# Kernel tuning notes

Hardware: AMD Instinct MI355X
Metric: run time of the kernel (lower is better)

Reference implementation:

```python
import jax, jax.numpy as jnp
import numpy as np

N_NODES = 50000


def gcn_conv(x, src, dst, W, b, n_nodes):
    # PyG GCNConv: add self-loops, symmetric normalization D^-1/2 (A+I) D^-1/2 (x W) + b
    E = src.shape[0]
    deg = jax.ops.segment_sum(jnp.ones((E,), x.dtype), dst, num_segments=n_nodes) + 1.0
    dinv = jax.lax.rsqrt(deg)
    h = x @ W  # [N, H]
    norm = dinv[src] * dinv[dst]  # [E]
    agg = jax.ops.segment_sum(h[src] * norm[:, None], dst, num_segments=n_nodes)
    agg = agg + h * (dinv * dinv)[:, None]  # self-loop contribution
    return agg + b


def setup_inputs() -> dict:
    key = jax.random.key(0)
    ks = jax.random.split(key, 16)
    N, E, D, H, T, O = N_NODES, 800000, 128, 128, 2, 1
    x = jax.random.normal(ks[0], (N, D), jnp.float32)
    edge_index = jax.random.randint(ks[1], (2, E), 0, N, jnp.int32)
    edge_attrs = jax.random.uniform(ks[2], (T, E, 7), jnp.float32)
    s = lambda k, sh: jax.random.normal(k, sh, jnp.float32) * (1.0 / np.sqrt(sh[0]))
    return {
        "x": x, "edge_index": edge_index, "edge_attrs": edge_attrs,
        "W1": s(ks[3], (D, H)), "b1": jnp.zeros((H,), jnp.float32),
        "W2": s(ks[4], (H, H)), "b2": jnp.zeros((H,), jnp.float32),
        "W3": s(ks[5], (H, H)), "b3": jnp.zeros((H,), jnp.float32),
        "We": s(ks[6], (2 * H + 7, H)), "be": jnp.zeros((H,), jnp.float32),
        "Wg": s(ks[7], (H, O)), "bg": jnp.zeros((O,), jnp.float32),
    }


def reference(x, edge_index, edge_attrs, W1, b1, W2, b2, W3, b3, We, be, Wg, bg):
    src, dst = edge_index[0], edge_index[1]
    n = x.shape[0]
    outputs = []
    for t in range(edge_attrs.shape[0]):  # small fixed T, x evolves across iterations
        edge_attr = edge_attrs[t]
        x = jax.nn.relu(gcn_conv(x, src, dst, W1, b1, n))
        x = jax.nn.relu(gcn_conv(x, src, dst, W2, b2, n))
        x = jax.nn.relu(gcn_conv(x, src, dst, W3, b3, n))
        # gather-concat-MLP-mean per edge
        edge_features = jnp.concatenate([x[src], x[dst], edge_attr], axis=1)
        edge_output = jax.nn.relu(edge_features @ We + be)
        graph_features = jnp.mean(edge_output, axis=0, keepdims=True)  # [1, H]
        outputs.append(graph_features @ Wg + bg)
        W1 = W2  # no-op placeholder removed below
        W1 = W1  # keep W1 unchanged
    return jnp.concatenate(outputs, axis=0)  # [T, output_dim]
```

## Files before the change

kernel.cpp:

```cpp
#include <hip/hip_runtime.h>
#include <hip/hip_bf16.h>


typedef __attribute__((ext_vector_type(8))) short bf16x8;
typedef __attribute__((ext_vector_type(4))) float f32x4;
typedef __attribute__((ext_vector_type(2))) float f32x2;

__device__ __forceinline__ unsigned short f2bf(float f) {
    union { float f; unsigned int u; } v; v.f = f;
    unsigned int r = v.u + 0x7fffu + ((v.u >> 16) & 1u);
    return (unsigned short)(r >> 16);
}
__device__ __forceinline__ float bf2f(unsigned short h) {
    union { unsigned int u; float f; } v; v.u = ((unsigned int)h) << 16;
    return v.f;
}
__device__ __forceinline__ unsigned int pk2bf(float lo, float hi) {
    return (unsigned int)f2bf(lo) | ((unsigned int)f2bf(hi) << 16);
}
__device__ __forceinline__ unsigned char f2fp8(float f) {
    return (unsigned char)(__builtin_amdgcn_cvt_pk_fp8_f32(f, f, 0, false) & 0xff);
}
__device__ __forceinline__ void fp8x4(unsigned int u, float* o) {
    f32x2 lo = __builtin_amdgcn_cvt_pk_f32_fp8(u, false);
    f32x2 hi = __builtin_amdgcn_cvt_pk_f32_fp8(u, true);
    o[0] = lo[0]; o[1] = lo[1]; o[2] = hi[0]; o[3] = hi[1];
}
__device__ __forceinline__ void de16add(uint4 v, float* a) {
    float t[4];
    fp8x4(v.x, t); a[0]+=t[0]; a[1]+=t[1]; a[2]+=t[2]; a[3]+=t[3];
    fp8x4(v.y, t); a[4]+=t[0]; a[5]+=t[1]; a[6]+=t[2]; a[7]+=t[3];
    fp8x4(v.z, t); a[8]+=t[0]; a[9]+=t[1]; a[10]+=t[2]; a[11]+=t[3];
    fp8x4(v.w, t); a[12]+=t[0]; a[13]+=t[1]; a[14]+=t[2]; a[15]+=t[3];
}

__global__ void to_bf16(const float* __restrict__ in, unsigned short* __restrict__ out, int n4)
{
    int i = blockIdx.x * 256 + threadIdx.x;
    if (i < n4) {
        float4 v = ((const float4*)in)[i];
        ushort4 o;
        o.x = f2bf(v.x); o.y = f2bf(v.y); o.z = f2bf(v.z); o.w = f2bf(v.w);
        ((ushort4*)out)[i] = o;
    }
}

__global__ void transpose_w(
    const float* __restrict__ W1, const float* __restrict__ W2,
    const float* __restrict__ W3, const float* __restrict__ We,
    unsigned short* __restrict__ T1, unsigned short* __restrict__ T2,
    unsigned short* __restrict__ T3, unsigned short* __restrict__ Tuv)
{
    const float* src; unsigned short* dst;
    switch (blockIdx.y) {
        case 0:  src = W1;             dst = T1;              break;
        case 1:  src = W2;             dst = T2;              break;
        case 2:  src = W3;             dst = T3;              break;
        case 3:  src = We;             dst = Tuv;             break;
        default: src = We + 128 * 128; dst = Tuv + 128 * 128; break;
    }
    for (int i = blockIdx.x * 256 + threadIdx.x; i < 128 * 128; i += 256 * gridDim.x) {
        int k = i >> 7, c = i & 127;
        dst[c * 128 + k] = f2bf(src[i]);
    }
}

__global__ __launch_bounds__(256) void mfma_matmul(
    const unsigned short* __restrict__ X, const unsigned short* __restrict__ Wt,
    unsigned char* __restrict__ out, const float* __restrict__ scale,
    int n_rows, int out_stride, int out_off)
{
    if (blockIdx.y) { Wt += 128 * 128; out_off += 128; }

    const int wave = threadIdx.x >> 6;
    const int lane = threadIdx.x & 63;
    const int m = lane & 15;
    const int q = lane >> 4;
    const int r = blockIdx.x * 64 + wave * 16 + m;
    const bool rv = r < n_rows;

    f32x4 acc[8];
    #pragma unroll
    for (int i = 0; i < 8; ++i) acc[i] = (f32x4){0.f, 0.f, 0.f, 0.f};

    #pragma unroll
    for (int k0 = 0; k0 < 128; k0 += 32) {
        bf16x8 a = {};
        if (rv) a = *(const bf16x8*)(X + (size_t)r * 128 + k0 + q * 8);
        #pragma unroll
        for (int ct = 0; ct < 8; ++ct) {
            bf16x8 b = *(const bf16x8*)(Wt + (ct * 16 + m) * 128 + k0 + q * 8);
            acc[ct] = __builtin_amdgcn_mfma_f32_16x16x32_bf16(a, b, acc[ct], 0, 0, 0);
        }
    }

    #pragma unroll
    for (int reg = 0; reg < 4; ++reg) {
        int gr = blockIdx.x * 64 + wave * 16 + q * 4 + reg;
        if (gr >= n_rows) continue;
        float s = scale ? scale[gr] : 1.0f;
        #pragma unroll
        for (int ct = 0; ct < 8; ++ct) {
            out[(size_t)gr * out_stride + out_off + ct * 16 + m] =
                f2fp8(acc[ct][reg] * s);
        }
    }
}

__global__ __launch_bounds__(256) void gcn_gather(
    const unsigned char* __restrict__ hs, const int* __restrict__ csr_src,
    const int* __restrict__ offs, const int* __restrict__ counts,
    const float* __restrict__ dinv, const float* __restrict__ bias,
    unsigned short* __restrict__ xout, int n)
{
    int node = blockIdx.x * 32 + (threadIdx.x >> 3);
    if (node >= n) return;
    int lane = threadIdx.x & 7;
    int c16 = lane * 16;
    int off = offs[node];
    int cnt = counts[node];

    float a[16] = {};
    de16add(*(const uint4*)(hs + (size_t)node * 128 + c16), a);

    int j = 0;
    for (; j + 8 <= cnt; j += 8) {
        int s0 = csr_src[off + j + 0];
        int s1 = csr_src[off + j + 1];
        int s2 = csr_src[off + j + 2];
        int s3 = csr_src[off + j + 3];
        int s4 = csr_src[off + j + 4];
        int s5 = csr_src[off + j + 5];
        int s6 = csr_src[off + j + 6];
        int s7 = csr_src[off + j + 7];
        uint4 h0 = *(const uint4*)(hs + (size_t)s0 * 128 + c16);
        uint4 h1 = *(const uint4*)(hs + (size_t)s1 * 128 + c16);
        uint4 h2 = *(const uint4*)(hs + (size_t)s2 * 128 + c16);
        uint4 h3 = *(const uint4*)(hs + (size_t)s3 * 128 + c16);
        uint4 h4 = *(const uint4*)(hs + (size_t)s4 * 128 + c16);
        uint4 h5 = *(const uint4*)(hs + (size_t)s5 * 128 + c16);
        uint4 h6 = *(const uint4*)(hs + (size_t)s6 * 128 + c16);
        uint4 h7 = *(const uint4*)(hs + (size_t)s7 * 128 + c16);
        de16add(h0, a); de16add(h1, a); de16add(h2, a); de16add(h3, a);
        de16add(h4, a); de16add(h5, a); de16add(h6, a); de16add(h7, a);
    }
    for (; j + 4 <= cnt; j += 4) {
        int s0 = csr_src[off + j + 0];
        int s1 = csr_src[off + j + 1];
        int s2 = csr_src[off + j + 2];
        int s3 = csr_src[off + j + 3];
        uint4 h0 = *(const uint4*)(hs + (size_t)s0 * 128 + c16);
        uint4 h1 = *(const uint4*)(hs + (size_t)s1 * 128 + c16);
        uint4 h2 = *(const uint4*)(hs + (size_t)s2 * 128 + c16);
        uint4 h3 = *(const uint4*)(hs + (size_t)s3 * 128 + c16);
        de16add(h0, a); de16add(h1, a); de16add(h2, a); de16add(h3, a);
    }
    for (; j < cnt; ++j) {
        int s = csr_src[off + j];
        de16add(*(const uint4*)(hs + (size_t)s * 128 + c16), a);
    }

    float dn = dinv[node];
    float r[16];
    #pragma unroll
    for (int i = 0; i < 4; ++i) {
        float4 bb = *(const float4*)(bias + c16 + i * 4);
        r[i*4+0] = fmaxf(fmaf(a[i*4+0], dn, bb.x), 0.f);
        r[i*4+1] = fmaxf(fmaf(a[i*4+1], dn, bb.y), 0.f);
        r[i*4+2] = fmaxf(fmaf(a[i*4+2], dn, bb.z), 0.f);
        r[i*4+3] = fmaxf(fmaf(a[i*4+3], dn, bb.w), 0.f);
    }
    uint4 o0, o1;
    o0.x = pk2bf(r[0], r[1]);  o0.y = pk2bf(r[2], r[3]);
    o0.z = pk2bf(r[4], r[5]);  o0.w = pk2bf(r[6], r[7]);
    o1.x = pk2bf(r[8], r[9]);  o1.y = pk2bf(r[10], r[11]);
    o1.z = pk2bf(r[12], r[13]); o1.w = pk2bf(r[14], r[15]);
    *(uint4*)(xout + (size_t)node * 128 + c16) = o0;
    *(uint4*)(xout + (size_t)node * 128 + c16 + 8) = o1;
}

#define EM_CHUNK 256
__global__ __launch_bounds__(256) void edge_mlp(
    const unsigned char* __restrict__ uv, const int* __restrict__ src,
    const int* __restrict__ dst, const float* __restrict__ ea,
    const float* __restrict__ We_e, const float* __restrict__ be,
    const float* __restrict__ Wg, float* __restrict__ acc, int E)
{
    const int tid  = threadIdx.x;
    const int lane = tid & 31;
    const int g    = tid >> 5;
    const int c4   = lane * 4;

    __shared__ float eas[EM_CHUNK * 7];
    __shared__ int   ss[EM_CHUNK];
    __shared__ int   ds[EM_CHUNK];
    __shared__ float red[256];

    float4 w[7];
    #pragma unroll
    for (int i = 0; i < 7; ++i)
        w[i] = *(const float4*)(We_e + i * 128 + c4);
    const float4 be4 = *(const float4*)(be + c4);
    const float4 wg4 = *(const float4*)(Wg + c4);

    float4 part = make_float4(0.f, 0.f, 0.f, 0.f);

    for (int base = blockIdx.x * EM_CHUNK; base < E; base += gridDim.x * EM_CHUNK) {
        const int nch = min(EM_CHUNK, E - base);
        for (int i = tid; i < nch * 7; i += 256)
            eas[i] = ea[(size_t)base * 7 + i];
        for (int i = tid; i < nch; i += 256) {
            ss[i] = src[base + i];
            ds[i] = dst[base + i];
        }
        __syncthreads();

        auto ev = [&](int j) {
            unsigned int us = *(const unsigned int*)(uv + (size_t)ss[j] * 256 + c4);
            unsigned int vs = *(const unsigned int*)(uv + (size_t)ds[j] * 256 + 128 + c4);
            float uf[4], vf[4];
            fp8x4(us, uf); fp8x4(vs, vf);
            const float* eav = &eas[j * 7];
            float4 val;
            val.x = uf[0] + vf[0] + be4.x;
            val.y = uf[1] + vf[1] + be4.y;
            val.z = uf[2] + vf[2] + be4.z;
            val.w = uf[3] + vf[3] + be4.w;
            #pragma unroll
            for (int i = 0; i < 7; ++i) {
                float e = eav[i];
                val.x = fmaf(e, w[i].x, val.x);
                val.y = fmaf(e, w[i].y, val.y);
                val.z = fmaf(e, w[i].z, val.z);
                val.w = fmaf(e, w[i].w, val.w);
            }
            part.x += fmaxf(val.x, 0.f);
            part.y += fmaxf(val.y, 0.f);
            part.z += fmaxf(val.z, 0.f);
            part.w += fmaxf(val.w, 0.f);
        };

        int j = g;
        for (; j + 32 <= nch; j += 32) {
            ev(j); ev(j + 8); ev(j + 16); ev(j + 24);
        }
        for (; j < nch; j += 8)
            ev(j);
        __syncthreads();
    }

    float p = part.x * wg4.x + part.y * wg4.y + part.z * wg4.z + part.w * wg4.w;
    red[tid] = p;
    __syncthreads();
    for (int s = 128; s > 0; s >>= 1) {
        if (tid < s) red[tid] += red[tid + s];
        __syncthreads();
    }
    if (tid == 0) atomicAdd(acc, red[0]);
}

__global__ void count_edges(const int* __restrict__ dst, int* __restrict__ counts, int E)
{
    int e = blockIdx.x * 256 + threadIdx.x;
    if (e < E) atomicAdd(&counts[dst[e]], 1);
}

__global__ void compute_dinv(const int* __restrict__ counts, float* __restrict__ dinv, int n)
{
    int i = blockIdx.x * 256 + threadIdx.x;
    if (i < n) dinv[i] = rsqrtf((float)counts[i] + 1.0f);
}

__global__ void scan1(const int* __restrict__ counts, int* __restrict__ scanned,
                      int* __restrict__ btot, int n)
{
    __shared__ int sh[256];
    int i = blockIdx.x * 256 + threadIdx.x;
    int v = (i < n) ? counts[i] : 0;
    sh[threadIdx.x] = v;
    __syncthreads();
    for (int off = 1; off < 256; off <<= 1) {
        int t = (threadIdx.x >= off) ? sh[threadIdx.x - off] : 0;
        __syncthreads();
        sh[threadIdx.x] += t;
        __syncthreads();
    }
    if (i < n) scanned[i] = sh[threadIdx.x] - v;
    if (threadIdx.x == 255) btot[blockIdx.x] = sh[255];
}

__global__ void scan2(int* __restrict__ btot, int nb)
{
    __shared__ int sh[256];
    int v = (threadIdx.x < nb) ? btot[threadIdx.x] : 0;
    sh[threadIdx.x] = v;
    __syncthreads();
    for (int off = 1; off < 256; off <<= 1) {
        int t = (threadIdx.x >= off) ? sh[threadIdx.x - off] : 0;
        __syncthreads();
        sh[threadIdx.x] += t;
        __syncthreads();
    }
    if (threadIdx.x < nb) btot[threadIdx.x] = sh[threadIdx.x] - v;
}

__global__ void scan3(const int* __restrict__ scanned, const int* __restrict__ btot,
                      int* __restrict__ offs, int* __restrict__ cursor, int n)
{
    int i = blockIdx.x * 256 + threadIdx.x;
    if (i < n) {
        int o = scanned[i] + btot[blockIdx.x];
        offs[i] = o;
        cursor[i] = o;
    }
}

__global__ void fill_csr(const int* __restrict__ src, const int* __restrict__ dst,
                         int* __restrict__ cursor, int* __restrict__ csr_src, int E)
{
    int e = blockIdx.x * 256 + threadIdx.x;
    if (e < E) {
        int slot = atomicAdd(&cursor[dst[e]], 1);
        csr_src[slot] = src[e];
    }
}

__global__ void write_out(const float* __restrict__ acc, const float* __restrict__ bg,
                          float* __restrict__ out, float invE, int T)
{
    int t = threadIdx.x;
    if (t < T) out[t] = acc[t] * invE + bg[0];
}


extern "C" void kernel_launch(void* const* d_in, const int* in_sizes, int n_in,
                              void* d_out, int out_size, void* d_ws, size_t ws_size,
                              hipStream_t stream)
{
    const float* x   = (const float*)d_in[0];
    const int*  eidx = (const int*)d_in[1];
    const float* ea  = (const float*)d_in[2];
    const float* W1  = (const float*)d_in[3];
    const float* b1  = (const float*)d_in[4];
    const float* W2  = (const float*)d_in[5];
    const float* b2  = (const float*)d_in[6];
    const float* W3  = (const float*)d_in[7];
    const float* b3  = (const float*)d_in[8];
    const float* We  = (const float*)d_in[9];
    const float* be  = (const float*)d_in[10];
    const float* Wg  = (const float*)d_in[11];
    const float* bg  = (const float*)d_in[12];

    const int N = in_sizes[0] / 128;
    const int E = in_sizes[1] / 2;
    const int T = in_sizes[2] / (E * 7);
    const int* src = eidx;
    const int* dst = eidx + E;

    char* wsp = (char*)d_ws;
    auto alloc = [&](size_t bytes) -> char* {
        char* p = wsp;
        wsp += (bytes + 255) / 256 * 256;
        return p;
    };
    int*   counts  = (int*)alloc((size_t)N * 4);
    int*   offs    = (int*)alloc((size_t)N * 4);
    int*   cursor  = (int*)alloc((size_t)N * 4);
    int*   scanned = (int*)alloc((size_t)N * 4);
    int*   btot    = (int*)alloc(1024);
    int*   csr_src = (int*)alloc((size_t)E * 4);
    float* dinv    = (float*)alloc((size_t)N * 4);
    float* acc     = (float*)alloc(256);
    unsigned short* X0 = (unsigned short*)alloc((size_t)N * 128 * 2);
    unsigned short* A  = (unsigned short*)alloc((size_t)N * 128 * 2);
    unsigned char*  B  = (unsigned char*)alloc((size_t)N * 256);
    unsigned short* T1 = (unsigned short*)alloc(128 * 128 * 2);
    unsigned short* T2 = (unsigned short*)alloc(128 * 128 * 2);
    unsigned short* T3 = (unsigned short*)alloc(128 * 128 * 2);
    unsigned short* Tuv = (unsigned short*)alloc(256 * 128 * 2);

    hipMemsetAsync(counts, 0, (size_t)N * 4, stream);
    hipMemsetAsync(acc, 0, (size_t)T * 4, stream);

    to_bf16<<<(N * 128 / 4 + 255) / 256, 256, 0, stream>>>(x, X0, N * 128 / 4);
    transpose_w<<<dim3(4, 5), 256, 0, stream>>>(W1, W2, W3, We, T1, T2, T3, Tuv);

    count_edges<<<(E + 255) / 256, 256, 0, stream>>>(dst, counts, E);
    compute_dinv<<<(N + 255) / 256, 256, 0, stream>>>(counts, dinv, N);
    const int nb = (N + 255) / 256;
    scan1<<<nb, 256, 0, stream>>>(counts, scanned, btot, N);
    scan2<<<1, 256, 0, stream>>>(btot, nb);
    scan3<<<nb, 256, 0, stream>>>(scanned, btot, offs, cursor, N);
    fill_csr<<<(E + 255) / 256, 256, 0, stream>>>(src, dst, cursor, csr_src, E);

    const int mmb = (N + 63) / 64;
    const int ngb = (N + 31) / 32;
    const int emb = (E + EM_CHUNK - 1) / EM_CHUNK;

    for (int t = 0; t < T; ++t) {
        const unsigned short* xin = (t == 0) ? X0 : A;
        const unsigned short* Tc1 = (t == 0) ? T1 : T2;
        mfma_matmul<<<dim3(mmb, 1), 256, 0, stream>>>(xin, Tc1, B, dinv, N, 128, 0);
        gcn_gather<<<ngb, 256, 0, stream>>>(B, csr_src, offs, counts, dinv, b1, A, N);
        mfma_matmul<<<dim3(mmb, 1), 256, 0, stream>>>(A, T2, B, dinv, N, 128, 0);
        gcn_gather<<<ngb, 256, 0, stream>>>(B, csr_src, offs, counts, dinv, b2, A, N);
        mfma_matmul<<<dim3(mmb, 1), 256, 0, stream>>>(A, T3, B, dinv, N, 128, 0);
        gcn_gather<<<ngb, 256, 0, stream>>>(B, csr_src, offs, counts, dinv, b3, A, N);
        mfma_matmul<<<dim3(mmb, 2), 256, 0, stream>>>(A, Tuv, B, nullptr, N, 256, 0);
        edge_mlp<<<emb, 256, 0, stream>>>(B, src, dst, ea + (size_t)t * E * 7,
                                          We + 256 * 128, be, Wg, acc + t, E);
    }
    write_out<<<1, 64, 0, stream>>>(acc, bg, (float*)d_out, 1.0f / (float)E, T);
}
```

Before: 671.6 us.

## Fuse GCN gather with the next layer's matmul via shared-memory tile

Each GCN aggregation kernel now writes its bf16 activations for a 64-node tile into LDS and immediately multiplies by the next layer's weights with MFMA. This removes the bf16 activation round trip through global memory and cuts the separate matmul launches. The third layer also computes the next timestep's first-layer projection alongside the edge projections, using an extended weight buffer that holds a W2 copy. The trade-offs are lower gather parallelism per block (64 nodes per block, each thread handling two nodes), an MFMA loop that reloads weights for each column tile, and fewer independent waves hiding gather latency.

```diff
diff --git a/kernel.cpp b/kernel.cpp
--- a/kernel.cpp
+++ b/kernel.cpp
@@ -10,10 +10,6 @@
     union { float f; unsigned int u; } v; v.f = f;
     unsigned int r = v.u + 0x7fffu + ((v.u >> 16) & 1u);
     return (unsigned short)(r >> 16);
-}
-__device__ __forceinline__ float bf2f(unsigned short h) {
-    union { unsigned int u; float f; } v; v.u = ((unsigned int)h) << 16;
-    return v.f;
 }
 __device__ __forceinline__ unsigned int pk2bf(float lo, float hi) {
     return (unsigned int)f2bf(lo) | ((unsigned int)f2bf(hi) << 16);
@@ -53,11 +49,12 @@
 {
     const float* src; unsigned short* dst;
     switch (blockIdx.y) {
-        case 0:  src = W1;             dst = T1;              break;
-        case 1:  src = W2;             dst = T2;              break;
-        case 2:  src = W3;             dst = T3;              break;
-        case 3:  src = We;             dst = Tuv;             break;
-        default: src = We + 128 * 128; dst = Tuv + 128 * 128; break;
+        case 0:  src = W1;             dst = T1;               break;
+        case 1:  src = W2;             dst = T2;               break;
+        case 2:  src = W3;             dst = T3;               break;
+        case 3:  src = We;             dst = Tuv;              break;
+        case 4:  src = We + 128 * 128; dst = Tuv + 128 * 128;  break;
+        default: src = W2;             dst = Tuv + 256 * 128;  break;
     }
     for (int i = blockIdx.x * 256 + threadIdx.x; i < 128 * 128; i += 256 * gridDim.x) {
         int k = i >> 7, c = i & 127;
@@ -67,11 +64,8 @@
 
 __global__ __launch_bounds__(256) void mfma_matmul(
     const unsigned short* __restrict__ X, const unsigned short* __restrict__ Wt,
-    unsigned char* __restrict__ out, const float* __restrict__ scale,
-    int n_rows, int out_stride, int out_off)
-{
-    if (blockIdx.y) { Wt += 128 * 128; out_off += 128; }
-
+    unsigned char* __restrict__ out, const float* __restrict__ scale, int n_rows)
+{
     const int wave = threadIdx.x >> 6;
     const int lane = threadIdx.x & 63;
     const int m = lane & 15;
@@ -98,85 +92,92 @@
     for (int reg = 0; reg < 4; ++reg) {
         int gr = blockIdx.x * 64 + wave * 16 + q * 4 + reg;
         if (gr >= n_rows) continue;
-        float s = scale ? scale[gr] : 1.0f;
+        float s = scale[gr];
         #pragma unroll
-        for (int ct = 0; ct < 8; ++ct) {
-            out[(size_t)gr * out_stride + out_off + ct * 16 + m] =
-                f2fp8(acc[ct][reg] * s);
-        }
-    }
-}
-
-__global__ __launch_bounds__(256) void gcn_gather(
-    const unsigned char* __restrict__ hs, const int* __restrict__ csr_src,
+        for (int ct = 0; ct < 8; ++ct)
+            out[(size_t)gr * 128 + ct * 16 + m] = f2fp8(acc[ct][reg] * s);
+    }
+}
+
+#define FPAD 136
+__global__ __launch_bounds__(256) void fused_gm(
+    const unsigned char* __restrict__ hs_in, const int* __restrict__ csr_src,
     const int* __restrict__ offs, const int* __restrict__ counts,
     const float* __restrict__ dinv, const float* __restrict__ bias,
-    unsigned short* __restrict__ xout, int n)
-{
-    int node = blockIdx.x * 32 + (threadIdx.x >> 3);
-    if (node >= n) return;
-    int lane = threadIdx.x & 7;
-    int c16 = lane * 16;
-    int off = offs[node];
-    int cnt = counts[node];
-
-    float a[16] = {};
-    de16add(*(const uint4*)(hs + (size_t)node * 128 + c16), a);
-
-    int j = 0;
-    for (; j + 8 <= cnt; j += 8) {
-        int s0 = csr_src[off + j + 0];
-        int s1 = csr_src[off + j + 1];
-        int s2 = csr_src[off + j + 2];
-        int s3 = csr_src[off + j + 3];
-        int s4 = csr_src[off + j + 4];
-        int s5 = csr_src[off + j + 5];
-        int s6 = csr_src[off + j + 6];
-        int s7 = csr_src[off + j + 7];
-        uint4 h0 = *(const uint4*)(hs + (size_t)s0 * 128 + c16);
-        uint4 h1 = *(const uint4*)(hs + (size_t)s1 * 128 + c16);
-        uint4 h2 = *(const uint4*)(hs + (size_t)s2 * 128 + c16);
-        uint4 h3 = *(const uint4*)(hs + (size_t)s3 * 128 + c16);
-        uint4 h4 = *(const uint4*)(hs + (size_t)s4 * 128 + c16);
-        uint4 h5 = *(const uint4*)(hs + (size_t)s5 * 128 + c16);
-        uint4 h6 = *(const uint4*)(hs + (size_t)s6 * 128 + c16);
-        uint4 h7 = *(const uint4*)(hs + (size_t)s7 * 128 + c16);
-        de16add(h0, a); de16add(h1, a); de16add(h2, a); de16add(h3, a);
-        de16add(h4, a); de16add(h5, a); de16add(h6, a); de16add(h7, a);
-    }
-    for (; j + 4 <= cnt; j += 4) {
-        int s0 = csr_src[off + j + 0];
-        int s1 = csr_src[off + j + 1];
-        int s2 = csr_src[off + j + 2];
-        int s3 = csr_src[off + j + 3];
-        uint4 h0 = *(const uint4*)(hs + (size_t)s0 * 128 + c16);
-        uint4 h1 = *(const uint4*)(hs + (size_t)s1 * 128 + c16);
-        uint4 h2 = *(const uint4*)(hs + (size_t)s2 * 128 + c16);
-        uint4 h3 = *(const uint4*)(hs + (size_t)s3 * 128 + c16);
-        de16add(h0, a); de16add(h1, a); de16add(h2, a); de16add(h3, a);
-    }
-    for (; j < cnt; ++j) {
-        int s = csr_src[off + j];
-        de16add(*(const uint4*)(hs + (size_t)s * 128 + c16), a);
-    }
-
-    float dn = dinv[node];
-    float r[16];
+    const unsigned short* __restrict__ Wt, int ncols, int uvcols,
+    unsigned char* __restrict__ buv, unsigned char* __restrict__ bh, int n)
+{
+    __shared__ unsigned short xs[64 * FPAD];
+    const int tid = threadIdx.x;
+
     #pragma unroll
-    for (int i = 0; i < 4; ++i) {
-        float4 bb = *(const float4*)(bias + c16 + i * 4);
-        r[i*4+0] = fmaxf(fmaf(a[i*4+0], dn, bb.x), 0.f);
-        r[i*4+1] = fmaxf(fmaf(a[i*4+1], dn, bb.y), 0.f);
-        r[i*4+2] = fmaxf(fmaf(a[i*4+2], dn, bb.z), 0.f);
-        r[i*4+3] = fmaxf(fmaf(a[i*4+3], dn, bb.w), 0.f);
-    }
-    uint4 o0, o1;
-    o0.x = pk2bf(r[0], r[1]);  o0.y = pk2bf(r[2], r[3]);
-    o0.z = pk2bf(r[4], r[5]);  o0.w = pk2bf(r[6], r[7]);
-    o1.x = pk2bf(r[8], r[9]);  o1.y = pk2bf(r[10], r[11]);
-    o1.z = pk2bf(r[12], r[13]); o1.w = pk2bf(r[14], r[15]);
-    *(uint4*)(xout + (size_t)node * 128 + c16) = o0;
-    *(uint4*)(xout + (size_t)node * 128 + c16 + 8) = o1;
+    for (int half = 0; half < 2; ++half) {
+        int row  = half * 32 + (tid >> 3);
+        int node = blockIdx.x * 64 + row;
+        if (node < n) {
+            int c16 = (tid & 7) * 16;
+            int off = offs[node];
+            int cnt = counts[node];
+
+            float a[16] = {};
+            de16add(*(const uint4*)(hs_in + (size_t)node * 128 + c16), a);
+            int j = 0;
+            for (; j + 4 <= cnt; j += 4) {
+                int s0 = csr_src[off + j + 0];
+                int s1 = csr_src[off + j + 1];
+                int s2 = csr_src[off + j + 2];
+                int s3 = csr_src[off + j + 3];
+                uint4 h0 = *(const uint4*)(hs_in + (size_t)s0 * 128 + c16);
+                uint4 h1 = *(const uint4*)(hs_in + (size_t)s1 * 128 + c16);
+                uint4 h2 = *(const uint4*)(hs_in + (size_t)s2 * 128 + c16);
+                uint4 h3 = *(const uint4*)(hs_in + (size_t)s3 * 128 + c16);
+                de16add(h0, a); de16add(h1, a); de16add(h2, a); de16add(h3, a);
+            }
+            for (; j < cnt; ++j) {
+                int s = csr_src[off + j];
+                de16add(*(const uint4*)(hs_in + (size_t)s * 128 + c16), a);
+            }
+
+            float dn = dinv[node];
+            #pragma unroll
+            for (int i = 0; i < 4; ++i) {
+                float4 bb = *(const float4*)(bias + c16 + i * 4);
+                float r0 = fmaxf(fmaf(a[i*4+0], dn, bb.x), 0.f);
+                float r1 = fmaxf(fmaf(a[i*4+1], dn, bb.y), 0.f);
+                float r2 = fmaxf(fmaf(a[i*4+2], dn, bb.z), 0.f);
+                float r3 = fmaxf(fmaf(a[i*4+3], dn, bb.w), 0.f);
+                *(unsigned int*)&xs[row * FPAD + c16 + i*4 + 0] = pk2bf(r0, r1);
+                *(unsigned int*)&xs[row * FPAD + c16 + i*4 + 2] = pk2bf(r2, r3);
+            }
+        }
+    }
+    __syncthreads();
+
+    const int wave = tid >> 6;
+    const int lane = tid & 63;
+    const int m = lane & 15;
+    const int q = lane >> 4;
+    const int nct = ncols >> 4;
+
+    for (int ct = 0; ct < nct; ++ct) {
+        f32x4 acc = (f32x4){0.f, 0.f, 0.f, 0.f};
+        #pragma unroll
+        for (int k0 = 0; k0 < 128; k0 += 32) {
+            bf16x8 a = *(const bf16x8*)&xs[(wave * 16 + m) * FPAD + k0 + q * 8];
+            bf16x8 b = *(const bf16x8*)(Wt + (size_t)(ct * 16 + m) * 128 + k0 + q * 8);
+            acc = __builtin_amdgcn_mfma_f32_16x16x32_bf16(a, b, acc, 0, 0, 0);
+        }
+        int col = ct * 16 + m;
+        #pragma unroll
+        for (int reg = 0; reg < 4; ++reg) {
+            int node = blockIdx.x * 64 + wave * 16 + q * 4 + reg;
+            if (node >= n) continue;
+            if (col < uvcols)
+                buv[(size_t)node * 256 + col] = f2fp8(acc[reg]);
+            else
+                bh[(size_t)node * 128 + col - uvcols] = f2fp8(acc[reg] * dinv[node]);
+        }
+    }
 }
 
 #define EM_CHUNK 256
@@ -371,19 +372,20 @@
     int*   csr_src = (int*)alloc((size_t)E * 4);
     float* dinv    = (float*)alloc((size_t)N * 4);
     float* acc     = (float*)alloc(256);
-    unsigned short* X0 = (unsigned short*)alloc((size_t)N * 128 * 2);
-    unsigned short* A  = (unsigned short*)alloc((size_t)N * 128 * 2);
-    unsigned char*  B  = (unsigned char*)alloc((size_t)N * 256);
-    unsigned short* T1 = (unsigned short*)alloc(128 * 128 * 2);
-    unsigned short* T2 = (unsigned short*)alloc(128 * 128 * 2);
-    unsigned short* T3 = (unsigned short*)alloc(128 * 128 * 2);
-    unsigned short* Tuv = (unsigned short*)alloc(256 * 128 * 2);
+    unsigned short* X0  = (unsigned short*)alloc((size_t)N * 128 * 2);
+    unsigned char*  Bh0 = (unsigned char*)alloc((size_t)N * 128);
+    unsigned char*  Bh1 = (unsigned char*)alloc((size_t)N * 128);
+    unsigned char*  Buv = (unsigned char*)alloc((size_t)N * 256);
+    unsigned short* T1  = (unsigned short*)alloc(128 * 128 * 2);
+    unsigned short* T2  = (unsigned short*)alloc(128 * 128 * 2);
+    unsigned short* T3  = (unsigned short*)alloc(128 * 128 * 2);
+    unsigned short* Tuv = (unsigned short*)alloc(384 * 128 * 2);
 
     hipMemsetAsync(counts, 0, (size_t)N * 4, stream);
     hipMemsetAsync(acc, 0, (size_t)T * 4, stream);
 
     to_bf16<<<(N * 128 / 4 + 255) / 256, 256, 0, stream>>>(x, X0, N * 128 / 4);
-    transpose_w<<<dim3(4, 5), 256, 0, stream>>>(W1, W2, W3, We, T1, T2, T3, Tuv);
+    transpose_w<<<dim3(8, 6), 256, 0, stream>>>(W1, W2, W3, We, T1, T2, T3, Tuv);
 
     count_edges<<<(E + 255) / 256, 256, 0, stream>>>(dst, counts, E);
     compute_dinv<<<(N + 255) / 256, 256, 0, stream>>>(counts, dinv, N);
@@ -394,20 +396,27 @@
     fill_csr<<<(E + 255) / 256, 256, 0, stream>>>(src, dst, cursor, csr_src, E);
 
     const int mmb = (N + 63) / 64;
-    const int ngb = (N + 31) / 32;
     const int emb = (E + EM_CHUNK - 1) / EM_CHUNK;
 
+    unsigned char* hcur = Bh0;
+    unsigned char* hnxt = Bh1;
+
     for (int t = 0; t < T; ++t) {
-        const unsigned short* xin = (t == 0) ? X0 : A;
-        const unsigned short* Tc1 = (t == 0) ? T1 : T2;
-        mfma_matmul<<<dim3(mmb, 1), 256, 0, stream>>>(xin, Tc1, B, dinv, N, 128, 0);
-        gcn_gather<<<ngb, 256, 0, stream>>>(B, csr_src, offs, counts, dinv, b1, A, N);
-        mfma_matmul<<<dim3(mmb, 1), 256, 0, stream>>>(A, T2, B, dinv, N, 128, 0);
-        gcn_gather<<<ngb, 256, 0, stream>>>(B, csr_src, offs, counts, dinv, b2, A, N);
-        mfma_matmul<<<dim3(mmb, 1), 256, 0, stream>>>(A, T3, B, dinv, N, 128, 0);
-        gcn_gather<<<ngb, 256, 0, stream>>>(B, csr_src, offs, counts, dinv, b3, A, N);
-        mfma_matmul<<<dim3(mmb, 2), 256, 0, stream>>>(A, Tuv, B, nullptr, N, 256, 0);
-        edge_mlp<<<emb, 256, 0, stream>>>(B, src, dst, ea + (size_t)t * E * 7,
+        if (t == 0) {
+            mfma_matmul<<<mmb, 256, 0, stream>>>(X0, T1, hcur, dinv, N);
+        }
+        fused_gm<<<mmb, 256, 0, stream>>>(hcur, csr_src, offs, counts, dinv, b1,
+                                          T2, 128, 0, Buv, hnxt, N);
+        { unsigned char* tmp = hcur; hcur = hnxt; hnxt = tmp; }
+        fused_gm<<<mmb, 256, 0, stream>>>(hcur, csr_src, offs, counts, dinv, b2,
+                                          T3, 128, 0, Buv, hnxt, N);
+        { unsigned char* tmp = hcur; hcur = hnxt; hnxt = tmp; }
+        bool last = (t == T - 1);
+        fused_gm<<<mmb, 256, 0, stream>>>(hcur, csr_src, offs, counts, dinv, b3,
+                                          Tuv, last ? 256 : 384, 256, Buv, hnxt, N);
+        if (!last) { unsigned char* tmp = hcur; hcur = hnxt; hnxt = tmp; }
+
+        edge_mlp<<<emb, 256, 0, stream>>>(Buv, src, dst, ea + (size_t)t * E * 7,
                                           We + 256 * 128, be, Wg, acc + t, E);
     }
     write_out<<<1, 64, 0, stream>>>(acc, bg, (float*)d_out, 1.0f / (float)E, T);
```

Result: faster. 613.5 us (-8.6%).
